# Performance work log

Measured on AMD Instinct MI355X. Metric: run time of the kernel, lower is better.

Reference implementation:

```python
import jax, jax.numpy as jnp
import numpy as np
import math

B, S, D = 4, 2048, 1024
WINDOW = 10  # window_size; attends to |i-j| <= WINDOW//2


def setup_inputs() -> dict:
    key = jax.random.key(0)
    ks = jax.random.split(key, 9)
    sc = 1.0 / math.sqrt(D)
    return {
        "x": jax.random.normal(ks[0], (B, S, D), dtype=jnp.float32),
        "Wq": jax.random.normal(ks[1], (D, D), dtype=jnp.float32) * sc,
        "bq": jnp.zeros((D,), dtype=jnp.float32),
        "Wk": jax.random.normal(ks[2], (D, D), dtype=jnp.float32) * sc,
        "bk": jnp.zeros((D,), dtype=jnp.float32),
        "Wv": jax.random.normal(ks[3], (D, D), dtype=jnp.float32) * sc,
        "bv": jnp.zeros((D,), dtype=jnp.float32),
        "Wo": jax.random.normal(ks[4], (D, D), dtype=jnp.float32) * sc,
        "bo": jnp.zeros((D,), dtype=jnp.float32),
    }


def _local_mask(seq_len: int, window_size: int) -> jnp.ndarray:
    # row i attends to columns [i - w//2, i + w//2] inclusive -> |i - j| <= w//2
    i = jnp.arange(seq_len)[:, None]
    j = jnp.arange(seq_len)[None, :]
    return jnp.abs(i - j) <= (window_size // 2)  # [S, S] bool


def reference(x, Wq, bq, Wk, bk, Wv, bv, Wo, bo):
    # nn.Linear: y = x @ W.T + b
    Q = x @ Wq.T + bq  # [B, S, D]
    K = x @ Wk.T + bk
    V = x @ Wv.T + bv
    scores = jnp.einsum("bqd,bkd->bqk", Q, K) / jnp.float32(math.sqrt(D))
    mask = _local_mask(x.shape[1], WINDOW)
    scores = jnp.where(mask[None, :, :], scores, jnp.float32(-1e9))
    attn = jax.nn.softmax(scores, axis=-1)  # [B, S, S]
    context = jnp.einsum("bqk,bkd->bqd", attn, V)
    output = context @ Wo.T + bo
    return output, attn
```

## Files before the change

kernel.cpp:

```cpp
#include <hip/hip_runtime.h>
#include <hip/hip_bf16.h>
#include <cstdint>
#include <cstddef>


typedef __attribute__((ext_vector_type(8))) short bf16x8;
typedef __attribute__((ext_vector_type(4))) float f32x4;
typedef __attribute__((ext_vector_type(8))) unsigned short ushortx8;

#define GPTR(x) ((const __attribute__((address_space(1))) void*)(x))
#define LPTR(x) ((__attribute__((address_space(3))) void*)(x))

__device__ __forceinline__ unsigned short f2bf(float f) {
    __hip_bfloat16 h = __float2bfloat16(f);
    unsigned short u;
    __builtin_memcpy(&u, &h, 2);
    return u;
}
__device__ __forceinline__ float bf2f(unsigned short u) {
    unsigned int x = ((unsigned int)u) << 16;
    float f;
    __builtin_memcpy(&f, &x, 4);
    return f;
}

__global__ void cvt_all(const float* __restrict__ x,
                        const float* __restrict__ Wq, const float* __restrict__ Wk,
                        const float* __restrict__ Wo,
                        unsigned short* __restrict__ xh,
                        unsigned short* __restrict__ Wcat,
                        unsigned short* __restrict__ Woh) {
    const int idx = blockIdx.x * blockDim.x + threadIdx.x;
    const float* src;
    unsigned short* dst;
    int s_off, d_off;
    if (idx < 2097152) {
        src = x; dst = xh; s_off = idx; d_off = idx;
    } else {
        const int r   = idx - 2097152;
        const int seg = r >> 18;
        const int off = r & 262143;
        src   = (seg == 0) ? Wq : (seg == 1) ? Wk : Wo;
        dst   = (seg < 2) ? Wcat : Woh;
        s_off = off;
        d_off = (seg < 2) ? (seg << 18) + off : off;
    }
    f32x4 v = reinterpret_cast<const f32x4*>(src)[s_off];
    ushort4 o;
    o.x = f2bf(v[0]); o.y = f2bf(v[1]); o.z = f2bf(v[2]); o.w = f2bf(v[3]);
    reinterpret_cast<ushort4*>(dst)[d_off] = o;
}

__global__ void transpose_cvt(const float* __restrict__ in,
                              unsigned short* __restrict__ out) {
    __shared__ float tl[64][65];
    const int t  = threadIdx.x;
    const int c  = t & 63;
    const int r4 = t >> 6;
    const int bx = blockIdx.x;
    const int by = blockIdx.y;
#pragma unroll
    for (int i = 0; i < 16; ++i) {
        const int r = r4 * 16 + i;
        tl[r][c] = in[(size_t)(by * 64 + r) * 1024 + bx * 64 + c];
    }
    __syncthreads();
#pragma unroll
    for (int i = 0; i < 16; ++i) {
        const int r = r4 * 16 + i;
        out[(size_t)(bx * 64 + r) * 1024 + by * 64 + c] = f2bf(tl[c][r]);
    }
}

__global__ void bvo_kernel(const float* __restrict__ Wo,
                           const float* __restrict__ bv,
                           float* __restrict__ bvo) {
    const int row  = blockIdx.x * 4 + (threadIdx.x >> 6);
    const int lane = threadIdx.x & 63;
    float s = 0.f;
#pragma unroll
    for (int k = lane; k < 1024; k += 64)
        s += Wo[(size_t)row * 1024 + k] * bv[k];
#pragma unroll
    for (int off = 32; off >= 1; off >>= 1) s += __shfl_xor(s, off, 64);
    if (lane == 0) bvo[row] = s;
}

__device__ __forceinline__ void gemm_core(const unsigned short* __restrict__ A,
                                          const unsigned short* __restrict__ Bw,
                                          int K, int tm, int tn,
                                          unsigned short* As, unsigned short* Bs,
                                          f32x4 (&acc)[4][4]) {
    const int tid  = threadIdx.x;
    const int lane = tid & 63;
    const int w    = tid >> 6;
    const int wr   = w >> 1;
    const int wc   = w & 1;

    const int lrow8 = lane >> 3;
    const int lcolb = (lane & 7) << 4;

    const char* Abase = (const char*)(A + (size_t)tm * 128 * (size_t)K);
    const char* Bbase = (const char*)(Bw + (size_t)tn * 128 * (size_t)K);
    const size_t rstride = (size_t)K * 2;

    const int nk = K >> 6;
    for (int t = 0; t < nk; ++t) {
        const size_t k0b = ((size_t)t << 6) * 2;
#pragma unroll
        for (int ii = 0; ii < 4; ++ii) {
            const int c    = (w << 2) + ii;
            const int row  = (c << 3) + lrow8;
            const int csrc = lcolb ^ ((row & 7) << 4);
            __builtin_amdgcn_global_load_lds(
                GPTR(Abase + (size_t)row * rstride + k0b + (size_t)csrc),
                LPTR((char*)As + (c << 10)), 16, 0, 0);
            __builtin_amdgcn_global_load_lds(
                GPTR(Bbase + (size_t)row * rstride + k0b + (size_t)csrc),
                LPTR((char*)Bs + (c << 10)), 16, 0, 0);
        }
        __syncthreads();

#pragma unroll
        for (int kk = 0; kk < 2; ++kk) {
            bf16x8 af[4], bfr[4];
            const int cb = (kk << 6) + ((lane >> 4) << 4);
#pragma unroll
            for (int m = 0; m < 4; ++m) {
                const int row = (wr << 6) + (m << 4) + (lane & 15);
                af[m] = *reinterpret_cast<const bf16x8*>(
                    (const char*)As + row * 128 + (cb ^ ((row & 7) << 4)));
            }
#pragma unroll
            for (int n = 0; n < 4; ++n) {
                const int row = (wc << 6) + (n << 4) + (lane & 15);
                bfr[n] = *reinterpret_cast<const bf16x8*>(
                    (const char*)Bs + row * 128 + (cb ^ ((row & 7) << 4)));
            }
#pragma unroll
            for (int m = 0; m < 4; ++m)
#pragma unroll
                for (int n = 0; n < 4; ++n)
                    acc[m][n] = __builtin_amdgcn_mfma_f32_16x16x32_bf16(
                        af[m], bfr[n], acc[m][n], 0, 0, 0);
        }
        __syncthreads();
    }
}

__launch_bounds__(256, 3)
__global__ void gemm_wp(const unsigned short* __restrict__ A,
                        const unsigned short* __restrict__ Bw,
                        unsigned short* __restrict__ C) {
    __shared__ unsigned short As[128 * 64];
    __shared__ unsigned short Bs[128 * 64];
    f32x4 acc[4][4];
#pragma unroll
    for (int m = 0; m < 4; ++m)
#pragma unroll
        for (int n = 0; n < 4; ++n) acc[m][n] = (f32x4){0.f, 0.f, 0.f, 0.f};

    const int sid = (blockIdx.x & 7) * 8 + (blockIdx.x >> 3);
    const int tm  = sid >> 3;
    const int tn  = sid & 7;

    gemm_core(A, Bw, 1024, tm, tn, As, Bs, acc);

    const int lane = threadIdx.x & 63;
    const int w    = threadIdx.x >> 6;
    const int wr   = w >> 1, wc = w & 1;
    const int col0 = (tn << 7) + (wc << 6) + (lane & 15);
    const int row0 = (tm << 7) + (wr << 6) + ((lane >> 4) << 2);
#pragma unroll
    for (int n = 0; n < 4; ++n) {
        const int col = col0 + (n << 4);
#pragma unroll
        for (int m = 0; m < 4; ++m) {
            const int row = row0 + (m << 4);
#pragma unroll
            for (int r = 0; r < 4; ++r)
                C[(size_t)(row + r) * 1024 + col] = f2bf(acc[m][n][r]);
        }
    }
}

__launch_bounds__(256, 3)
__global__ void gemm_qkv(const unsigned short* __restrict__ A,
                         const unsigned short* __restrict__ Bw,
                         const float* __restrict__ bq, const float* __restrict__ bk,
                         const float* __restrict__ bvo,
                         unsigned short* __restrict__ C, int M, int N, int K) {
    __shared__ unsigned short As[128 * 64];
    __shared__ unsigned short Bs[128 * 64];
    f32x4 acc[4][4];
#pragma unroll
    for (int m = 0; m < 4; ++m)
#pragma unroll
        for (int n = 0; n < 4; ++n) acc[m][n] = (f32x4){0.f, 0.f, 0.f, 0.f};

    const int ntn = N >> 7;
    const int sid = (blockIdx.x & 7) * (gridDim.x >> 3) + (blockIdx.x >> 3);
    const int tm  = sid / ntn;
    const int tn  = sid % ntn;

    gemm_core(A, Bw, K, tm, tn, As, Bs, acc);

    const int lane = threadIdx.x & 63;
    const int w    = threadIdx.x >> 6;
    const int wr   = w >> 1, wc = w & 1;
    const int seg  = tn >> 3;
    const float* bp = (seg == 0) ? bq : (seg == 1) ? bk : bvo;

    const int col0 = (tn << 7) + (wc << 6) + (lane & 15);
    const int row0 = (tm << 7) + (wr << 6) + ((lane >> 4) << 2);
#pragma unroll
    for (int n = 0; n < 4; ++n) {
        const int col = col0 + (n << 4);
        const float bb = bp[col & 1023];
#pragma unroll
        for (int m = 0; m < 4; ++m) {
            const int row = row0 + (m << 4);
#pragma unroll
            for (int r = 0; r < 4; ++r)
                C[(size_t)(row + r) * (size_t)N + col] = f2bf(acc[m][n][r] + bb);
        }
    }
}

__launch_bounds__(256, 4)
__global__ void attn_band_kernel(const unsigned short* __restrict__ QKV,
                                 const float* __restrict__ bo,
                                 float* __restrict__ attn,
                                 float* __restrict__ outp) {
    __shared__ float psm[4][16];
    const int bid  = blockIdx.x;
    const int rb   = (bid & 7) * 256 + (bid >> 3);
    const int w    = threadIdx.x >> 6;
    const int lane = threadIdx.x & 63;
    const int g    = (rb << 2) + w;
    const int b    = g >> 11;
    const int i    = g & 2047;

    const unsigned short* qrow = QKV + (size_t)g * 3072;
    float qf[16];
    {
        ushortx8 qa = *reinterpret_cast<const ushortx8*>(qrow + (lane << 4));
        ushortx8 qb = *reinterpret_cast<const ushortx8*>(qrow + (lane << 4) + 8);
#pragma unroll
        for (int t = 0; t < 8; ++t) { qf[t] = bf2f(qa[t]); qf[8 + t] = bf2f(qb[t]); }
    }

    float s[11];
#pragma unroll
    for (int jj = 0; jj < 11; ++jj) {
        const int j = i - 5 + jj;
        const bool valid = ((unsigned)j < 2048u);
        const int jc = min(max(j, 0), 2047);
        const unsigned short* krow = QKV + ((size_t)(b << 11) + jc) * 3072 + 1024;
        ushortx8 ka = *reinterpret_cast<const ushortx8*>(krow + (lane << 4));
        ushortx8 kb = *reinterpret_cast<const ushortx8*>(krow + (lane << 4) + 8);
        float d = 0.f;
#pragma unroll
        for (int t = 0; t < 8; ++t)
            d += qf[t] * bf2f(ka[t]) + qf[8 + t] * bf2f(kb[t]);
#pragma unroll
        for (int off = 32; off >= 1; off >>= 1) d += __shfl_xor(d, off, 64);
        s[jj] = valid ? d * 0.03125f : -1e30f;
    }

    float mx = s[0];
#pragma unroll
    for (int jj = 1; jj < 11; ++jj) mx = fmaxf(mx, s[jj]);
    float p[11], sum = 0.f;
#pragma unroll
    for (int jj = 0; jj < 11; ++jj) { p[jj] = expf(s[jj] - mx); sum += p[jj]; }
    const float inv = 1.0f / sum;

    if (lane == 0) {
#pragma unroll
        for (int jj = 0; jj < 11; ++jj) psm[w][jj] = p[jj] * inv;
    }
    __syncthreads();

    const int lo = i - 5;
    float* arow = attn + (size_t)g * 2048;
#pragma unroll
    for (int e = 0; e < 8; ++e) {
        const int c0 = (e << 8) + (lane << 2);
        f32x4 v = (f32x4){0.f, 0.f, 0.f, 0.f};
        if (c0 + 3 >= lo && c0 <= lo + 10) {
#pragma unroll
            for (int t = 0; t < 4; ++t) {
                const int d = c0 + t - lo;
                if ((unsigned)d < 11u) v[t] = psm[w][d];
            }
        }
        *reinterpret_cast<f32x4*>(arow + c0) = v;
    }

    float cacc[16];
#pragma unroll
    for (int t = 0; t < 16; ++t) cacc[t] = 0.f;
#pragma unroll
    for (int jj = 0; jj < 11; ++jj) {
        const int j  = i - 5 + jj;
        const int jc = min(max(j, 0), 2047);
        const float pj = p[jj] * inv;
        const unsigned short* vrow = QKV + ((size_t)(b << 11) + jc) * 3072 + 2048;
        ushortx8 va = *reinterpret_cast<const ushortx8*>(vrow + (lane << 4));
        ushortx8 vb = *reinterpret_cast<const ushortx8*>(vrow + (lane << 4) + 8);
#pragma unroll
        for (int t = 0; t < 8; ++t) {
            cacc[t]     += pj * bf2f(va[t]);
            cacc[8 + t] += pj * bf2f(vb[t]);
        }
    }
    const int c0 = lane << 4;
    float* op = outp + (size_t)g * 1024 + c0;
#pragma unroll
    for (int q = 0; q < 4; ++q) {
        f32x4 bb = *reinterpret_cast<const f32x4*>(bo + c0 + (q << 2));
        f32x4 o;
#pragma unroll
        for (int t = 0; t < 4; ++t) o[t] = cacc[(q << 2) + t] + bb[t];
        *reinterpret_cast<f32x4*>(op + (q << 2)) = o;
    }
}

extern "C" void kernel_launch(void* const* d_in, const int* in_sizes, int n_in,
                              void* d_out, int out_size, void* d_ws, size_t ws_size,
                              hipStream_t stream) {
    const float* x  = (const float*)d_in[0];
    const float* Wq = (const float*)d_in[1];
    const float* bq = (const float*)d_in[2];
    const float* Wk = (const float*)d_in[3];
    const float* bk = (const float*)d_in[4];
    const float* Wv = (const float*)d_in[5];
    const float* bv = (const float*)d_in[6];
    const float* Wo = (const float*)d_in[7];
    const float* bo = (const float*)d_in[8];

    const size_t MS = 8192, DD = 1024;

    float* out  = (float*)d_out;
    float* attn = out + MS * DD;

    char* ws = (char*)d_ws;
    unsigned short* xh   = (unsigned short*)ws; ws += MS * DD * 2;
    unsigned short* Wcat = (unsigned short*)ws; ws += 3 * DD * DD * 2;
    unsigned short* Woh  = (unsigned short*)ws; ws += DD * DD * 2;
    unsigned short* Wvt  = (unsigned short*)ws; ws += DD * DD * 2;
    float*          bvo  = (float*)ws;          ws += DD * 4;
    unsigned short* QKV  = (unsigned short*)ws; ws += MS * 3 * DD * 2;

    bvo_kernel<<<dim3(256), dim3(256), 0, stream>>>(Wo, bv, bvo);
    transpose_cvt<<<dim3(16, 16), dim3(256), 0, stream>>>(Wv, Wvt);
    cvt_all<<<dim3(11264), dim3(256), 0, stream>>>(x, Wq, Wk, Wo, xh, Wcat, Woh);

    gemm_wp<<<dim3(64), dim3(256), 0, stream>>>(Woh, Wvt, Wcat + 2 * DD * DD);

    gemm_qkv<<<dim3(1536), dim3(256), 0, stream>>>(xh, Wcat, bq, bk, bvo,
                                                   QKV, 8192, 3072, 1024);

    attn_band_kernel<<<dim3(2048), dim3(256), 0, stream>>>(QKV, bo, attn, out);
}
```

Baseline: 132.8 us.

## Fold Wq^T Wk into a single weight product to shrink the big GEMM

Scores are rewritten algebraically as x_i·(Wq^T Wk) x_j plus bias terms. The combined D×D weight Wq^T Wk is precomputed with a split-K GEMM alongside the existing Wo·Wv fold, so the main GEMM produces 2048 columns (y and V') instead of 3072 (Q, K, V). Bias cross terms are handled by new small kernels computing per-row scalars r1 and r2. This removes a third of the large GEMM's FLOPs and output traffic. In exchange it adds several extra kernels, a float partial buffer and a reduction, and the scores now use a bf16-rounded product matrix, which changes rounding.

```diff
diff --git a/kernel.cpp b/kernel.cpp
--- a/kernel.cpp
+++ b/kernel.cpp
@@ -24,51 +24,28 @@
     return f;
 }
 
-__global__ void cvt_all(const float* __restrict__ x,
-                        const float* __restrict__ Wq, const float* __restrict__ Wk,
-                        const float* __restrict__ Wo,
-                        unsigned short* __restrict__ xh,
-                        unsigned short* __restrict__ Wcat,
-                        unsigned short* __restrict__ Woh) {
-    const int idx = blockIdx.x * blockDim.x + threadIdx.x;
-    const float* src;
-    unsigned short* dst;
-    int s_off, d_off;
-    if (idx < 2097152) {
-        src = x; dst = xh; s_off = idx; d_off = idx;
-    } else {
-        const int r   = idx - 2097152;
-        const int seg = r >> 18;
-        const int off = r & 262143;
-        src   = (seg == 0) ? Wq : (seg == 1) ? Wk : Wo;
-        dst   = (seg < 2) ? Wcat : Woh;
-        s_off = off;
-        d_off = (seg < 2) ? (seg << 18) + off : off;
-    }
-    f32x4 v = reinterpret_cast<const f32x4*>(src)[s_off];
-    ushort4 o;
-    o.x = f2bf(v[0]); o.y = f2bf(v[1]); o.z = f2bf(v[2]); o.w = f2bf(v[3]);
-    reinterpret_cast<ushort4*>(dst)[d_off] = o;
-}
-
-__global__ void transpose_cvt(const float* __restrict__ in,
-                              unsigned short* __restrict__ out) {
-    __shared__ float tl[64][65];
-    const int t  = threadIdx.x;
-    const int c  = t & 63;
-    const int r4 = t >> 6;
-    const int bx = blockIdx.x;
-    const int by = blockIdx.y;
-#pragma unroll
-    for (int i = 0; i < 16; ++i) {
-        const int r = r4 * 16 + i;
-        tl[r][c] = in[(size_t)(by * 64 + r) * 1024 + bx * 64 + c];
-    }
-    __syncthreads();
-#pragma unroll
-    for (int i = 0; i < 16; ++i) {
-        const int r = r4 * 16 + i;
-        out[(size_t)(bx * 64 + r) * 1024 + by * 64 + c] = f2bf(tl[c][r]);
+__global__ void w_kernel(const float* __restrict__ bq, const float* __restrict__ bk,
+                         const float* __restrict__ Wq, const float* __restrict__ Wk,
+                         float* __restrict__ w1, float* __restrict__ w2,
+                         float* __restrict__ cbuf) {
+    const int d = blockIdx.x * 256 + threadIdx.x;
+    float a1 = 0.f, a2 = 0.f;
+    for (int n = 0; n < 1024; ++n) {
+        a1 += bq[n] * Wk[(size_t)n * 1024 + d];
+        a2 += bk[n] * Wq[(size_t)n * 1024 + d];
+    }
+    w1[d] = a1; w2[d] = a2;
+    if (blockIdx.x == 0) {
+        __shared__ float red[256];
+        float pc = 0.f;
+        for (int n = threadIdx.x; n < 1024; n += 256) pc += bq[n] * bk[n];
+        red[threadIdx.x] = pc;
+        __syncthreads();
+        for (int s = 128; s > 0; s >>= 1) {
+            if (threadIdx.x < s) red[threadIdx.x] += red[threadIdx.x + s];
+            __syncthreads();
+        }
+        if (threadIdx.x == 0) cbuf[0] = red[0];
     }
 }
 
@@ -86,9 +63,78 @@
     if (lane == 0) bvo[row] = s;
 }
 
+__global__ void cvt_all(const float* __restrict__ x, const float* __restrict__ Wo,
+                        unsigned short* __restrict__ xh,
+                        unsigned short* __restrict__ Woh) {
+    const int idx = blockIdx.x * blockDim.x + threadIdx.x;
+    const float* src;
+    unsigned short* dst;
+    int off;
+    if (idx < 2097152) { src = x;  dst = xh;  off = idx; }
+    else               { src = Wo; dst = Woh; off = idx - 2097152; }
+    f32x4 v = reinterpret_cast<const f32x4*>(src)[off];
+    ushort4 o;
+    o.x = f2bf(v[0]); o.y = f2bf(v[1]); o.z = f2bf(v[2]); o.w = f2bf(v[3]);
+    reinterpret_cast<ushort4*>(dst)[off] = o;
+}
+
+__global__ void transpose_cvt3(const float* __restrict__ Wq,
+                               const float* __restrict__ Wk,
+                               const float* __restrict__ Wv,
+                               unsigned short* __restrict__ Wqt,
+                               unsigned short* __restrict__ Wkt,
+                               unsigned short* __restrict__ Wvt) {
+    __shared__ float tl[64][65];
+    const float* in = (blockIdx.z == 0) ? Wq : (blockIdx.z == 1) ? Wk : Wv;
+    unsigned short* out = (blockIdx.z == 0) ? Wqt : (blockIdx.z == 1) ? Wkt : Wvt;
+    const int t  = threadIdx.x;
+    const int c  = t & 63;
+    const int r4 = t >> 6;
+    const int bx = blockIdx.x;
+    const int by = blockIdx.y;
+#pragma unroll
+    for (int i = 0; i < 16; ++i) {
+        const int r = r4 * 16 + i;
+        tl[r][c] = in[(size_t)(by * 64 + r) * 1024 + bx * 64 + c];
+    }
+    __syncthreads();
+#pragma unroll
+    for (int i = 0; i < 16; ++i) {
+        const int r = r4 * 16 + i;
+        out[(size_t)(bx * 64 + r) * 1024 + by * 64 + c] = f2bf(tl[c][r]);
+    }
+}
+
+__launch_bounds__(256, 4)
+__global__ void r12_kernel(const unsigned short* __restrict__ xh,
+                           const float* __restrict__ w1, const float* __restrict__ w2,
+                           const float* __restrict__ cbuf,
+                           float* __restrict__ r1, float* __restrict__ r2) {
+    const int w    = threadIdx.x >> 6;
+    const int lane = threadIdx.x & 63;
+    const int g    = blockIdx.x * 4 + w;
+    const unsigned short* row = xh + (size_t)g * 1024 + (lane << 4);
+    ushortx8 xa = *reinterpret_cast<const ushortx8*>(row);
+    ushortx8 xb = *reinterpret_cast<const ushortx8*>(row + 8);
+    float a1 = 0.f, a2 = 0.f;
+#pragma unroll
+    for (int t = 0; t < 8; ++t) {
+        const float xv = bf2f(xa[t]);
+        const float xw = bf2f(xb[t]);
+        a1 += xv * w1[(lane << 4) + t] + xw * w1[(lane << 4) + 8 + t];
+        a2 += xv * w2[(lane << 4) + t] + xw * w2[(lane << 4) + 8 + t];
+    }
+#pragma unroll
+    for (int off = 32; off >= 1; off >>= 1) {
+        a1 += __shfl_xor(a1, off, 64);
+        a2 += __shfl_xor(a2, off, 64);
+    }
+    if (lane == 0) { r1[g] = a1 + cbuf[0]; r2[g] = a2; }
+}
+
 __device__ __forceinline__ void gemm_core(const unsigned short* __restrict__ A,
                                           const unsigned short* __restrict__ Bw,
-                                          int K, int tm, int tn,
+                                          int Kstride, int nk, int tm, int tn,
                                           unsigned short* As, unsigned short* Bs,
                                           f32x4 (&acc)[4][4]) {
     const int tid  = threadIdx.x;
@@ -100,11 +146,10 @@
     const int lrow8 = lane >> 3;
     const int lcolb = (lane & 7) << 4;
 
-    const char* Abase = (const char*)(A + (size_t)tm * 128 * (size_t)K);
-    const char* Bbase = (const char*)(Bw + (size_t)tn * 128 * (size_t)K);
-    const size_t rstride = (size_t)K * 2;
-
-    const int nk = K >> 6;
+    const char* Abase = (const char*)(A + (size_t)tm * 128 * (size_t)Kstride);
+    const char* Bbase = (const char*)(Bw + (size_t)tn * 128 * (size_t)Kstride);
+    const size_t rstride = (size_t)Kstride * 2;
+
     for (int t = 0; t < nk; ++t) {
         const size_t k0b = ((size_t)t << 6) * 2;
 #pragma unroll
@@ -149,9 +194,11 @@
 }
 
 __launch_bounds__(256, 3)
-__global__ void gemm_wp(const unsigned short* __restrict__ A,
-                        const unsigned short* __restrict__ Bw,
-                        unsigned short* __restrict__ C) {
+__global__ void gemm_splitk(const unsigned short* __restrict__ Wqt,
+                            const unsigned short* __restrict__ Wkt,
+                            const unsigned short* __restrict__ Woh,
+                            const unsigned short* __restrict__ Wvt,
+                            float* __restrict__ part) {
     __shared__ unsigned short As[128 * 64];
     __shared__ unsigned short Bs[128 * 64];
     f32x4 acc[4][4];
@@ -160,12 +207,19 @@
 #pragma unroll
         for (int n = 0; n < 4; ++n) acc[m][n] = (f32x4){0.f, 0.f, 0.f, 0.f};
 
-    const int sid = (blockIdx.x & 7) * 8 + (blockIdx.x >> 3);
-    const int tm  = sid >> 3;
-    const int tn  = sid & 7;
-
-    gemm_core(A, Bw, 1024, tm, tn, As, Bs, acc);
-
+    const int bid = blockIdx.x;
+    const int mat = bid >> 8;
+    const int loc = bid & 255;
+    const int ks  = loc >> 6;
+    const int t64 = loc & 63;
+    const int tm  = t64 >> 3;
+    const int tn  = t64 & 7;
+
+    const unsigned short* A = mat ? Woh : Wqt;
+    const unsigned short* B = mat ? Wvt : Wkt;
+    gemm_core(A + ks * 256, B + ks * 256, 1024, 4, tm, tn, As, Bs, acc);
+
+    float* dst = part + ((size_t)(mat * 4 + ks) << 20);
     const int lane = threadIdx.x & 63;
     const int w    = threadIdx.x >> 6;
     const int wr   = w >> 1, wc = w & 1;
@@ -179,17 +233,31 @@
             const int row = row0 + (m << 4);
 #pragma unroll
             for (int r = 0; r < 4; ++r)
-                C[(size_t)(row + r) * 1024 + col] = f2bf(acc[m][n][r]);
-        }
-    }
-}
-
-__launch_bounds__(256, 3)
-__global__ void gemm_qkv(const unsigned short* __restrict__ A,
-                         const unsigned short* __restrict__ Bw,
-                         const float* __restrict__ bq, const float* __restrict__ bk,
-                         const float* __restrict__ bvo,
-                         unsigned short* __restrict__ C, int M, int N, int K) {
+                dst[(size_t)(row + r) * 1024 + col] = acc[m][n][r];
+        }
+    }
+}
+
+__global__ void reduce_wp(const float* __restrict__ part,
+                          unsigned short* __restrict__ W2) {
+    const int u = blockIdx.x * 256 + threadIdx.x;
+    const int mat = u >> 18;
+    const int off = u & 262143;
+    const f32x4* p = reinterpret_cast<const f32x4*>(part);
+    f32x4 s = p[((size_t)(mat * 4 + 0) << 18) + off];
+    s += p[((size_t)(mat * 4 + 1) << 18) + off];
+    s += p[((size_t)(mat * 4 + 2) << 18) + off];
+    s += p[((size_t)(mat * 4 + 3) << 18) + off];
+    ushort4 o;
+    o.x = f2bf(s[0]); o.y = f2bf(s[1]); o.z = f2bf(s[2]); o.w = f2bf(s[3]);
+    reinterpret_cast<ushort4*>(W2)[u] = o;
+}
+
+__launch_bounds__(256, 4)
+__global__ void gemm_yv(const unsigned short* __restrict__ A,
+                        const unsigned short* __restrict__ Bw,
+                        const float* __restrict__ bvo,
+                        unsigned short* __restrict__ C) {
     __shared__ unsigned short As[128 * 64];
     __shared__ unsigned short Bs[128 * 64];
     f32x4 acc[4][4];
@@ -198,37 +266,37 @@
 #pragma unroll
         for (int n = 0; n < 4; ++n) acc[m][n] = (f32x4){0.f, 0.f, 0.f, 0.f};
 
-    const int ntn = N >> 7;
     const int sid = (blockIdx.x & 7) * (gridDim.x >> 3) + (blockIdx.x >> 3);
-    const int tm  = sid / ntn;
-    const int tn  = sid % ntn;
-
-    gemm_core(A, Bw, K, tm, tn, As, Bs, acc);
+    const int tm  = sid >> 4;
+    const int tn  = sid & 15;
+
+    gemm_core(A, Bw, 1024, 16, tm, tn, As, Bs, acc);
 
     const int lane = threadIdx.x & 63;
     const int w    = threadIdx.x >> 6;
     const int wr   = w >> 1, wc = w & 1;
     const int seg  = tn >> 3;
-    const float* bp = (seg == 0) ? bq : (seg == 1) ? bk : bvo;
-
     const int col0 = (tn << 7) + (wc << 6) + (lane & 15);
     const int row0 = (tm << 7) + (wr << 6) + ((lane >> 4) << 2);
 #pragma unroll
     for (int n = 0; n < 4; ++n) {
         const int col = col0 + (n << 4);
-        const float bb = bp[col & 1023];
+        const float bb = seg ? bvo[col & 1023] : 0.f;
 #pragma unroll
         for (int m = 0; m < 4; ++m) {
             const int row = row0 + (m << 4);
 #pragma unroll
             for (int r = 0; r < 4; ++r)
-                C[(size_t)(row + r) * (size_t)N + col] = f2bf(acc[m][n][r] + bb);
+                C[(size_t)(row + r) * 2048 + col] = f2bf(acc[m][n][r] + bb);
         }
     }
 }
 
 __launch_bounds__(256, 4)
-__global__ void attn_band_kernel(const unsigned short* __restrict__ QKV,
+__global__ void attn_band_kernel(const unsigned short* __restrict__ xh,
+                                 const unsigned short* __restrict__ yVp,
+                                 const float* __restrict__ r1,
+                                 const float* __restrict__ r2,
                                  const float* __restrict__ bo,
                                  float* __restrict__ attn,
                                  float* __restrict__ outp) {
@@ -241,7 +309,7 @@
     const int b    = g >> 11;
     const int i    = g & 2047;
 
-    const unsigned short* qrow = QKV + (size_t)g * 3072;
+    const unsigned short* qrow = xh + (size_t)g * 1024;
     float qf[16];
     {
         ushortx8 qa = *reinterpret_cast<const ushortx8*>(qrow + (lane << 4));
@@ -249,6 +317,7 @@
 #pragma unroll
         for (int t = 0; t < 8; ++t) { qf[t] = bf2f(qa[t]); qf[8 + t] = bf2f(qb[t]); }
     }
+    const float r2g = r2[g];
 
     float s[11];
 #pragma unroll
@@ -256,7 +325,8 @@
         const int j = i - 5 + jj;
         const bool valid = ((unsigned)j < 2048u);
         const int jc = min(max(j, 0), 2047);
-        const unsigned short* krow = QKV + ((size_t)(b << 11) + jc) * 3072 + 1024;
+        const int gj = (b << 11) + jc;
+        const unsigned short* krow = yVp + (size_t)gj * 2048;
         ushortx8 ka = *reinterpret_cast<const ushortx8*>(krow + (lane << 4));
         ushortx8 kb = *reinterpret_cast<const ushortx8*>(krow + (lane << 4) + 8);
         float d = 0.f;
@@ -265,7 +335,7 @@
             d += qf[t] * bf2f(ka[t]) + qf[8 + t] * bf2f(kb[t]);
 #pragma unroll
         for (int off = 32; off >= 1; off >>= 1) d += __shfl_xor(d, off, 64);
-        s[jj] = valid ? d * 0.03125f : -1e30f;
+        s[jj] = valid ? (d + r2g + r1[gj]) * 0.03125f : -1e30f;
     }
 
     float mx = s[0];
@@ -306,7 +376,7 @@
         const int j  = i - 5 + jj;
         const int jc = min(max(j, 0), 2047);
         const float pj = p[jj] * inv;
-        const unsigned short* vrow = QKV + ((size_t)(b << 11) + jc) * 3072 + 2048;
+        const unsigned short* vrow = yVp + ((size_t)((b << 11) + jc)) * 2048 + 1024;
         ushortx8 va = *reinterpret_cast<const ushortx8*>(vrow + (lane << 4));
         ushortx8 vb = *reinterpret_cast<const ushortx8*>(vrow + (lane << 4) + 8);
 #pragma unroll
@@ -347,20 +417,32 @@
 
     char* ws = (char*)d_ws;
     unsigned short* xh   = (unsigned short*)ws; ws += MS * DD * 2;
-    unsigned short* Wcat = (unsigned short*)ws; ws += 3 * DD * DD * 2;
     unsigned short* Woh  = (unsigned short*)ws; ws += DD * DD * 2;
+    unsigned short* Wqt  = (unsigned short*)ws; ws += DD * DD * 2;
+    unsigned short* Wkt  = (unsigned short*)ws; ws += DD * DD * 2;
     unsigned short* Wvt  = (unsigned short*)ws; ws += DD * DD * 2;
     float*          bvo  = (float*)ws;          ws += DD * 4;
-    unsigned short* QKV  = (unsigned short*)ws; ws += MS * 3 * DD * 2;
-
+    float*          w1   = (float*)ws;          ws += DD * 4;
+    float*          w2   = (float*)ws;          ws += DD * 4;
+    float*          cbuf = (float*)ws;          ws += 256;
+    float*          r1   = (float*)ws;          ws += MS * 4;
+    float*          r2   = (float*)ws;          ws += MS * 4;
+    float*          part = (float*)ws;          ws += (size_t)8 * DD * DD * 4;
+    unsigned short* W2   = (unsigned short*)ws; ws += 2 * DD * DD * 2;
+    unsigned short* yVp  = (unsigned short*)ws; ws += MS * 2 * DD * 2;
+
+    w_kernel<<<dim3(4), dim3(256), 0, stream>>>(bq, bk, Wq, Wk, w1, w2, cbuf);
     bvo_kernel<<<dim3(256), dim3(256), 0, stream>>>(Wo, bv, bvo);
-    transpose_cvt<<<dim3(16, 16), dim3(256), 0, stream>>>(Wv, Wvt);
-    cvt_all<<<dim3(11264), dim3(256), 0, stream>>>(x, Wq, Wk, Wo, xh, Wcat, Woh);
-
-    gemm_wp<<<dim3(64), dim3(256), 0, stream>>>(Woh, Wvt, Wcat + 2 * DD * DD);
-
-    gemm_qkv<<<dim3(1536), dim3(256), 0, stream>>>(xh, Wcat, bq, bk, bvo,
-                                                   QKV, 8192, 3072, 1024);
-
-    attn_band_kernel<<<dim3(2048), dim3(256), 0, stream>>>(QKV, bo, attn, out);
-}
+    cvt_all<<<dim3(9216), dim3(256), 0, stream>>>(x, Wo, xh, Woh);
+    transpose_cvt3<<<dim3(16, 16, 3), dim3(256), 0, stream>>>(Wq, Wk, Wv,
+                                                              Wqt, Wkt, Wvt);
+    r12_kernel<<<dim3(2048), dim3(256), 0, stream>>>(xh, w1, w2, cbuf, r1, r2);
+
+    gemm_splitk<<<dim3(512), dim3(256), 0, stream>>>(Wqt, Wkt, Woh, Wvt, part);
+    reduce_wp<<<dim3(2048), dim3(256), 0, stream>>>(part, W2);
+
+    gemm_yv<<<dim3(1024), dim3(256), 0, stream>>>(xh, W2, bvo, yVp);
+
+    attn_band_kernel<<<dim3(2048), dim3(256), 0, stream>>>(xh, yVp, r1, r2, bo,
+                                                           attn, out);
+}
```

Result: slower. 178.7 us (+34.6%).
